# Optimization experiments

Hardware: AMD Instinct MI355X
Metric: run time of the kernel (lower is better)

## Reference

```python
import jax, jax.numpy as jnp
import numpy as np

NUM_HEADS = 16


def setup_inputs() -> dict:
    key = jax.random.key(0)
    kx, kp, kq, kw, kb = jax.random.split(key, 5)
    B, N, C = 2, 2048, 1024
    x = jax.random.normal(kx, (B, N, C), dtype=jnp.float32)
    padding_mask = jax.random.randint(kp, (B, N), 0, 2).astype(jnp.bool_)
    W_qkv = jax.random.normal(kq, (C, 3 * C), dtype=jnp.float32) * (C ** -0.5)
    W_proj = jax.random.normal(kw, (C, C), dtype=jnp.float32) * (C ** -0.5)
    b_proj = jax.random.normal(kb, (C,), dtype=jnp.float32) * 0.02
    return {"x": x, "padding_mask": padding_mask, "causal_start": 128,
            "W_qkv": W_qkv, "W_proj": W_proj, "b_proj": b_proj}


def reference(x, padding_mask, causal_start, W_qkv, W_proj, b_proj):
    B, N, C = x.shape
    H = NUM_HEADS
    d = C // H
    scale = d ** -0.5
    # qkv projection: (B,N,3C) -> (3,B,H,N,d)
    qkv = (x @ W_qkv).reshape(B, N, 3, H, d).transpose(2, 0, 3, 1, 4)
    q, k, v = qkv[0], qkv[1], qkv[2]
    attn = jnp.einsum("bhqd,bhkd->bhqk", q * scale, k)  # (B,H,N,N)
    # padding mask: mask out padded KEY positions
    attn = jnp.where(padding_mask[:, None, None, :], -jnp.inf, attn)
    # offset causal mask: lower-triangular, but first `causal_start` columns always visible
    allowed = jnp.tril(jnp.ones((N, N), dtype=jnp.bool_))
    allowed = allowed | (jnp.arange(N)[None, :] < causal_start)
    attn = jnp.where(~allowed[None, None, :, :], -jnp.inf, attn)
    attn = jax.nn.softmax(attn.astype(jnp.float32), axis=-1).astype(x.dtype)
    out = jnp.einsum("bhqk,bhkd->bhqd", attn, v)  # (B,H,N,d)
    out = out.transpose(0, 2, 1, 3).reshape(B, N, C)
    return out @ W_proj + b_proj
```

## Files before the change

kernel.cpp:

```cpp
#include <hip/hip_runtime.h>
#include <stdint.h>

typedef unsigned short ushort_t;
typedef __attribute__((ext_vector_type(4))) unsigned short ushort4_t;
typedef __attribute__((ext_vector_type(8))) short short8;
typedef __attribute__((ext_vector_type(4))) float float4_t;

#define AS1 __attribute__((address_space(1)))
#define AS3 __attribute__((address_space(3)))

__device__ inline ushort_t f2bf(float f) {
    unsigned x = __builtin_bit_cast(unsigned, f);
    unsigned r = x + 0x7fffu + ((x >> 16) & 1u);
    return (ushort_t)(r >> 16);
}
__device__ inline ushort_t f2bf_trunc(float f) {
    return (ushort_t)(__builtin_bit_cast(unsigned, f) >> 16);
}

__global__ __launch_bounds__(256) void prep_fused(
    const float* __restrict__ wqkv, const float* __restrict__ x,
    ushort_t* __restrict__ wqkvT, ushort_t* __restrict__ xbf) {
    __shared__ __align__(16) ushort_t tile[64][65];
    int bid = blockIdx.x, t = threadIdx.x;
    if (bid < 768) {
        int bx = bid % 48, by = bid / 48;
        int c0 = bx * 64, r0 = by * 64;
        for (int i = 0; i < 16; i++) {
            int idx = t + i * 256;
            int lr = idx >> 6, lc = idx & 63;
            tile[lr][lc] = f2bf(wqkv[(size_t)(r0 + lr) * 3072 + c0 + lc]);
        }
        __syncthreads();
        for (int i = 0; i < 16; i++) {
            int idx = t + i * 256;
            int lr = idx >> 6, lc = idx & 63;
            wqkvT[(size_t)(c0 + lr) * 1024 + r0 + lc] = tile[lc][lr];
        }
    } else {
        size_t i = ((size_t)(bid - 768) * 256 + t) * 8;
        float4_t a = *(const float4_t*)(x + i);
        float4_t b = *(const float4_t*)(x + i + 4);
        ushort_t u[8];
        u[0] = f2bf(a.x); u[1] = f2bf(a.y); u[2] = f2bf(a.z); u[3] = f2bf(a.w);
        u[4] = f2bf(b.x); u[5] = f2bf(b.y); u[6] = f2bf(b.z); u[7] = f2bf(b.w);
        *(ushort4_t*)(xbf + i) = *(ushort4_t*)&u[0];
        *(ushort4_t*)(xbf + i + 4) = *(ushort4_t*)&u[4];
    }
}

__global__ __launch_bounds__(256) void transpose_f32_bf16(const float* __restrict__ in,
                                                          ushort_t* __restrict__ out,
                                                          int R, int C) {
    __shared__ __align__(16) ushort_t tile[64][65];
    int c0 = blockIdx.x * 64, r0 = blockIdx.y * 64;
    int t = threadIdx.x;
    for (int i = 0; i < 16; i++) {
        int idx = t + i * 256;
        int lr = idx >> 6, lc = idx & 63;
        tile[lr][lc] = f2bf(in[(size_t)(r0 + lr) * C + c0 + lc]);
    }
    __syncthreads();
    for (int i = 0; i < 16; i++) {
        int idx = t + i * 256;
        int lr = idx >> 6, lc = idx & 63;
        out[(size_t)(c0 + lr) * R + r0 + lc] = tile[lc][lr];
    }
}

__global__ __launch_bounds__(256) void gemm_qkv(
    const ushort_t* __restrict__ A, const ushort_t* __restrict__ Bt,
    ushort_t* __restrict__ outQ, ushort_t* __restrict__ outK, ushort_t* __restrict__ outV) {
    const int K = 1024;
    __shared__ __align__(16) ushort_t As[128 * 64];
    __shared__ __align__(16) ushort_t Bs[128 * 64];
    int t = threadIdx.x;
    int w = t >> 6, lane = t & 63;
    int quad = lane >> 4, l15 = lane & 15;
    int wM = w >> 1, wN = w & 1;
    int tM = blockIdx.y * 128, tN = blockIdx.x * 128;

    float4_t acc[4][4];
    for (int i = 0; i < 4; i++)
        for (int j = 0; j < 4; j++) acc[i][j] = (float4_t){0.f, 0.f, 0.f, 0.f};

    int lrow = lane >> 3;
    int lcol8 = (lane & 7) * 8;

    const ushort_t* Abase = A + (size_t)(tM + w * 32) * K;
    const ushort_t* Bbase = Bt + (size_t)(tN + w * 32) * K;

    for (int k0 = 0; k0 < K; k0 += 64) {
        __syncthreads();
        for (int i = 0; i < 4; i++) {
            const ushort_t* ga = Abase + (size_t)(i * 8 + lrow) * K + k0 + lcol8;
            __builtin_amdgcn_global_load_lds((AS1 void*)ga, (AS3 void*)&As[(w * 32 + i * 8) * 64], 16, 0, 0);
            const ushort_t* gb = Bbase + (size_t)(i * 8 + lrow) * K + k0 + lcol8;
            __builtin_amdgcn_global_load_lds((AS1 void*)gb, (AS3 void*)&Bs[(w * 32 + i * 8) * 64], 16, 0, 0);
        }
        __syncthreads();
        for (int kt = 0; kt < 2; kt++) {
            short8 af[4], bf[4];
            for (int m = 0; m < 4; m++)
                af[m] = *(const short8*)&As[(wM * 64 + m * 16 + l15) * 64 + kt * 32 + quad * 8];
            for (int n = 0; n < 4; n++)
                bf[n] = *(const short8*)&Bs[(wN * 64 + n * 16 + l15) * 64 + kt * 32 + quad * 8];
            for (int m = 0; m < 4; m++)
                for (int n = 0; n < 4; n++)
                    acc[m][n] = __builtin_amdgcn_mfma_f32_16x16x32_bf16(af[m], bf[n], acc[m][n], 0, 0, 0);
        }
    }

    for (int m = 0; m < 4; m++) {
        int gm = tM + wM * 64 + m * 16 + quad * 4;
        for (int n = 0; n < 4; n++) {
            int gn = tN + wN * 64 + n * 16 + l15;
            int three = gn >> 10;
            int h = (gn >> 6) & 15;
            int dd = gn & 63;
            ushort_t* dst = (three == 0) ? outQ : (three == 1) ? outK : outV;
            for (int r = 0; r < 4; r++) {
                int row = gm + r;
                int b = row >> 11;
                int ns = row & 2047;
                dst[(((size_t)(b * 16 + h) * 2048 + ns) << 6) + dd] = f2bf(acc[m][n][r]);
            }
        }
    }
}

__global__ __launch_bounds__(512, 4) void attn_kernel(
    const ushort_t* __restrict__ q, const ushort_t* __restrict__ k,
    const ushort_t* __restrict__ v, const int* __restrict__ pad,
    const int* __restrict__ csp, ushort_t* __restrict__ out) {
    __shared__ __align__(16) ushort_t Ks[2][64 * 64];
    __shared__ __align__(16) ushort_t VsT[2][64 * 64];
    __shared__ __align__(16) ushort_t Ps[8][16 * 64];
    __shared__ float padb[2048];

    int cs = csp[0];
    int t = threadIdx.x, w = t >> 6, lane = t & 63;
    int quad = lane >> 4, l15 = lane & 15;
    int bh = blockIdx.y;
    int b = bh >> 4, h = bh & 15;
    int g = (blockIdx.y < 16) ? blockIdx.x : 15 - blockIdx.x;
    int q0 = g * 128;
    int rowmin = q0 + w * 16;
    const float c1 = 0.18033688f;
    const float c2 = -11.541560f;

    for (int i = 0; i < 4; i++) {
        int key = t + i * 512;
        padb[key] = pad[b * 2048 + key] ? -1e38f : c2;
    }

    const ushort_t* qb = q + ((size_t)bh * 2048 + rowmin + l15) * 64;
    short8 qf0 = *(const short8*)(qb + quad * 8);
    short8 qf1 = *(const short8*)(qb + 32 + quad * 8);

    float4_t O[4];
    for (int i = 0; i < 4; i++) O[i] = (float4_t){0.f, 0.f, 0.f, 0.f};
    float ls[4] = {0.f, 0.f, 0.f, 0.f};

    int csT = (cs + 63) >> 6;
    int nT = 2 * g + 2;
    if (csT > nT) nT = csT;

    const ushort_t* kbase = k + (size_t)bh * 2048 * 64;
    const ushort_t* vbase = v + (size_t)bh * 2048 * 64;

    int lrow = lane >> 3, lblk = lane & 7;
    int prow = rowmin + quad * 4;
    int sw = l15 & 7;

    short8 vr;
    auto stageK = [&](int it, int buf) {
        int k0 = it * 64;
        const ushort_t* gk = kbase + (size_t)(k0 + w * 8 + lrow) * 64 + ((lblk ^ lrow) * 8);
        __builtin_amdgcn_global_load_lds((AS1 void*)gk, (AS3 void*)&Ks[buf][w * 8 * 64], 16, 0, 0);
    };
    auto loadV = [&](int it) {
        vr = *(const short8*)(vbase + (size_t)(it * 64 + lane) * 64 + w * 8);
    };

    stageK(0, 0);
    loadV(0);

    for (int it = 0; it < nT; it++) {
        int cur = it & 1, nxt = cur ^ 1;
        for (int j = 0; j < 8; j++) {
            int sl = ((lrow ^ j) * 8) + lblk;
            VsT[cur][(w * 8 + j) * 64 + sl] = (ushort_t)vr[j];
        }
        __syncthreads();
        if (it + 1 < nT) {
            stageK(it + 1, nxt);
            loadV(it + 1);
        }

        int k0 = it * 64;
        bool act = (k0 <= rowmin + 15) || (k0 < cs);
        if (act) {
            short8 kf0[4], kf1[4];
            for (int ks = 0; ks < 4; ks++) {
                const ushort_t* krow = &Ks[cur][(ks * 16 + l15) * 64];
                kf0[ks] = *(const short8*)(krow + (quad ^ sw) * 8);
                kf1[ks] = *(const short8*)(krow + ((4 + quad) ^ sw) * 8);
            }

            float4_t s[4];
            for (int ks = 0; ks < 4; ks++) {
                float4_t a = (float4_t){0.f, 0.f, 0.f, 0.f};
                a = __builtin_amdgcn_mfma_f32_16x16x32_bf16(qf0, kf0[ks], a, 0, 0, 0);
                a = __builtin_amdgcn_mfma_f32_16x16x32_bf16(qf1, kf1[ks], a, 0, 0, 0);
                s[ks] = a;
            }
            bool needC = (k0 + 63 > rowmin) && (k0 + 63 >= cs);
            for (int ks = 0; ks < 4; ks++) {
                int key = k0 + ks * 16 + l15;
                float add = padb[key];
                for (int r = 0; r < 4; r++) {
                    float arg = s[ks][r] * c1 + add;
                    if (needC && (key > prow + r) && (key >= cs)) arg = -1e38f;
                    float p = __builtin_amdgcn_exp2f(arg);
                    ls[r] += p;
                    int row = quad * 4 + r;
                    Ps[w][row * 64 + (((ks * 2 + (l15 >> 3)) ^ (row & 7)) * 8) + (l15 & 7)] = f2bf_trunc(p);
                }
            }

            short8 vf0[4], vf1[4];
            for (int n = 0; n < 4; n++) {
                const ushort_t* vrow = &VsT[cur][(n * 16 + l15) * 64];
                vf0[n] = *(const short8*)(vrow + (quad ^ sw) * 8);
                vf1[n] = *(const short8*)(vrow + ((4 + quad) ^ sw) * 8);
            }
            const ushort_t* prl = &Ps[w][l15 * 64];
            short8 pf0 = *(const short8*)(prl + (quad ^ sw) * 8);
            short8 pf1 = *(const short8*)(prl + ((4 + quad) ^ sw) * 8);
            for (int n = 0; n < 4; n++) {
                O[n] = __builtin_amdgcn_mfma_f32_16x16x32_bf16(pf0, vf0[n], O[n], 0, 0, 0);
                O[n] = __builtin_amdgcn_mfma_f32_16x16x32_bf16(pf1, vf1[n], O[n], 0, 0, 0);
            }
        }
    }

    for (int r = 0; r < 4; r++) {
        float l = ls[r];
        l += __shfl_xor(l, 1, 64); l += __shfl_xor(l, 2, 64);
        l += __shfl_xor(l, 4, 64); l += __shfl_xor(l, 8, 64);
        float inv = l > 0.f ? 1.f / l : 0.f;
        int row = rowmin + quad * 4 + r;
        size_t ob = ((size_t)b * 2048 + row) * 1024 + h * 64;
        for (int n = 0; n < 4; n++)
            out[ob + n * 16 + l15] = f2bf(O[n][r] * inv);
    }
}

__global__ __launch_bounds__(256) void gemm_out_k(
    const ushort_t* __restrict__ A, const ushort_t* __restrict__ Bt,
    const float* __restrict__ bias, float* __restrict__ outC) {
    const int K = 1024, N = 1024;
    __shared__ __align__(16) ushort_t As[128 * 64];
    __shared__ __align__(16) ushort_t Bs[128 * 64];
    int t = threadIdx.x;
    int w = t >> 6, lane = t & 63;
    int quad = lane >> 4, l15 = lane & 15;
    int wM = w >> 1, wN = w & 1;
    int tM = blockIdx.y * 128, tN = blockIdx.x * 128;

    float4_t acc[4][4];
    for (int i = 0; i < 4; i++)
        for (int j = 0; j < 4; j++) acc[i][j] = (float4_t){0.f, 0.f, 0.f, 0.f};

    int lrow = lane >> 3;
    int lcol8 = (lane & 7) * 8;

    const ushort_t* Abase = A + (size_t)(tM + w * 32) * K;
    const ushort_t* Bbase = Bt + (size_t)(tN + w * 32) * K;

    for (int k0 = 0; k0 < K; k0 += 64) {
        __syncthreads();
        for (int i = 0; i < 4; i++) {
            const ushort_t* ga = Abase + (size_t)(i * 8 + lrow) * K + k0 + lcol8;
            __builtin_amdgcn_global_load_lds((AS1 void*)ga, (AS3 void*)&As[(w * 32 + i * 8) * 64], 16, 0, 0);
            const ushort_t* gb = Bbase + (size_t)(i * 8 + lrow) * K + k0 + lcol8;
            __builtin_amdgcn_global_load_lds((AS1 void*)gb, (AS3 void*)&Bs[(w * 32 + i * 8) * 64], 16, 0, 0);
        }
        __syncthreads();
        for (int kt = 0; kt < 2; kt++) {
            short8 af[4], bf[4];
            for (int m = 0; m < 4; m++)
                af[m] = *(const short8*)&As[(wM * 64 + m * 16 + l15) * 64 + kt * 32 + quad * 8];
            for (int n = 0; n < 4; n++)
                bf[n] = *(const short8*)&Bs[(wN * 64 + n * 16 + l15) * 64 + kt * 32 + quad * 8];
            for (int m = 0; m < 4; m++)
                for (int n = 0; n < 4; n++)
                    acc[m][n] = __builtin_amdgcn_mfma_f32_16x16x32_bf16(af[m], bf[n], acc[m][n], 0, 0, 0);
        }
    }

    for (int m = 0; m < 4; m++) {
        int gm = tM + wM * 64 + m * 16 + quad * 4;
        for (int n = 0; n < 4; n++) {
            int gn = tN + wN * 64 + n * 16 + l15;
            float bv = bias[gn];
            for (int r = 0; r < 4; r++)
                outC[(size_t)(gm + r) * N + gn] = acc[m][n][r] + bv;
        }
    }
}

extern "C" void kernel_launch(void* const* d_in, const int* in_sizes, int n_in,
                              void* d_out, int out_size, void* d_ws, size_t ws_size,
                              hipStream_t stream) {
    const float* x = (const float*)d_in[0];
    const int* pad = (const int*)d_in[1];
    const int* cs = (const int*)d_in[2];
    const float* wqkv = (const float*)d_in[3];
    const float* wproj = (const float*)d_in[4];
    const float* bproj = (const float*)d_in[5];
    float* out = (float*)d_out;

    ushort_t* ws = (ushort_t*)d_ws;
    ushort_t* qws = ws;
    ushort_t* kws = ws + (size_t)4194304;
    ushort_t* vws = ws + (size_t)8388608;
    ushort_t* wqkvT = ws + (size_t)12582912;
    ushort_t* aows = ws + (size_t)12582912;
    ushort_t* wprojT = ws;
    ushort_t* xbf = (ushort_t*)d_out;

    prep_fused<<<2816, 256, 0, stream>>>(wqkv, x, wqkvT, xbf);
    gemm_qkv<<<dim3(24, 32), 256, 0, stream>>>(xbf, wqkvT, qws, kws, vws);
    attn_kernel<<<dim3(16, 32), 512, 0, stream>>>(qws, kws, vws, pad, cs, aows);
    transpose_f32_bf16<<<dim3(16, 16), 256, 0, stream>>>(wproj, wprojT, 1024, 1024);
    gemm_out_k<<<dim3(8, 32), 256, 0, stream>>>(aows, wprojT, bproj, out);
}
```

Before: 201.0 us.

## Split long causal attention rows across blocks with atomic accumulation and combine pass

Result: slower. 258.3 us (+28.5%).

```diff
diff --git a/kernel.cpp b/kernel.cpp
--- a/kernel.cpp
+++ b/kernel.cpp
@@ -129,30 +129,36 @@
     }
 }
 
-__global__ __launch_bounds__(512, 4) void attn_kernel(
+__global__ __launch_bounds__(512, 6) void attn_kernel(
     const ushort_t* __restrict__ q, const ushort_t* __restrict__ k,
     const ushort_t* __restrict__ v, const int* __restrict__ pad,
-    const int* __restrict__ csp, ushort_t* __restrict__ out) {
+    const int* __restrict__ csp, ushort_t* __restrict__ out,
+    float* __restrict__ Oacc, float* __restrict__ lsacc) {
     __shared__ __align__(16) ushort_t Ks[2][64 * 64];
     __shared__ __align__(16) ushort_t VsT[2][64 * 64];
     __shared__ __align__(16) ushort_t Ps[8][16 * 64];
-    __shared__ float padb[2048];
+
+    const int g_tab[24]  = {0,1,2,3,8,8,4,9, 15,13,12,10,10,11,9,5, 15,7,14,14,6,12,13,11};
+    const int t0_tab[24] = {0,0,0,0,0,9,0,10, 0,0,0,0,11,0,0,0,    16,0,0,15,0,13,14,12};
+    const int t1_tab[24] = {2,4,6,8,9,18,10,20, 16,14,13,11,22,12,10,12, 32,16,15,30,14,26,28,24};
 
     int cs = csp[0];
     int t = threadIdx.x, w = t >> 6, lane = t & 63;
     int quad = lane >> 4, l15 = lane & 15;
     int bh = blockIdx.y;
     int b = bh >> 4, h = bh & 15;
-    int g = (blockIdx.y < 16) ? blockIdx.x : 15 - blockIdx.x;
+    int xi = blockIdx.x;
+    int g = g_tab[xi];
+    int it0 = t0_tab[xi], it1 = t1_tab[xi];
+    bool split = (g >= 8);
     int q0 = g * 128;
     int rowmin = q0 + w * 16;
     const float c1 = 0.18033688f;
     const float c2 = -11.541560f;
 
-    for (int i = 0; i < 4; i++) {
-        int key = t + i * 512;
-        padb[key] = pad[b * 2048 + key] ? -1e38f : c2;
-    }
+    int csT = (cs + 63) >> 6;
+    bool lastitem = (g < 8) || (it0 > 0);
+    if (lastitem && csT > it1) it1 = csT;
 
     const ushort_t* qb = q + ((size_t)bh * 2048 + rowmin + l15) * 64;
     short8 qf0 = *(const short8*)(qb + quad * 8);
@@ -162,12 +168,9 @@
     for (int i = 0; i < 4; i++) O[i] = (float4_t){0.f, 0.f, 0.f, 0.f};
     float ls[4] = {0.f, 0.f, 0.f, 0.f};
 
-    int csT = (cs + 63) >> 6;
-    int nT = 2 * g + 2;
-    if (csT > nT) nT = csT;
-
     const ushort_t* kbase = k + (size_t)bh * 2048 * 64;
     const ushort_t* vbase = v + (size_t)bh * 2048 * 64;
+    const int* padp = pad + b * 2048;
 
     int lrow = lane >> 3, lblk = lane & 7;
     int prow = rowmin + quad * 4;
@@ -183,17 +186,17 @@
         vr = *(const short8*)(vbase + (size_t)(it * 64 + lane) * 64 + w * 8);
     };
 
-    stageK(0, 0);
-    loadV(0);
-
-    for (int it = 0; it < nT; it++) {
+    stageK(it0, it0 & 1);
+    loadV(it0);
+
+    for (int it = it0; it < it1; it++) {
         int cur = it & 1, nxt = cur ^ 1;
         for (int j = 0; j < 8; j++) {
             int sl = ((lrow ^ j) * 8) + lblk;
             VsT[cur][(w * 8 + j) * 64 + sl] = (ushort_t)vr[j];
         }
         __syncthreads();
-        if (it + 1 < nT) {
+        if (it + 1 < it1) {
             stageK(it + 1, nxt);
             loadV(it + 1);
         }
@@ -201,6 +204,9 @@
         int k0 = it * 64;
         bool act = (k0 <= rowmin + 15) || (k0 < cs);
         if (act) {
+            int pvv[4];
+            for (int ks = 0; ks < 4; ks++) pvv[ks] = padp[k0 + ks * 16 + l15];
+
             short8 kf0[4], kf1[4];
             for (int ks = 0; ks < 4; ks++) {
                 const ushort_t* krow = &Ks[cur][(ks * 16 + l15) * 64];
@@ -218,7 +224,7 @@
             bool needC = (k0 + 63 > rowmin) && (k0 + 63 >= cs);
             for (int ks = 0; ks < 4; ks++) {
                 int key = k0 + ks * 16 + l15;
-                float add = padb[key];
+                float add = pvv[ks] ? -1e38f : c2;
                 for (int r = 0; r < 4; r++) {
                     float arg = s[ks][r] * c1 + add;
                     if (needC && (key > prow + r) && (key >= cs)) arg = -1e38f;
@@ -245,16 +251,47 @@
         }
     }
 
-    for (int r = 0; r < 4; r++) {
-        float l = ls[r];
-        l += __shfl_xor(l, 1, 64); l += __shfl_xor(l, 2, 64);
-        l += __shfl_xor(l, 4, 64); l += __shfl_xor(l, 8, 64);
-        float inv = l > 0.f ? 1.f / l : 0.f;
-        int row = rowmin + quad * 4 + r;
-        size_t ob = ((size_t)b * 2048 + row) * 1024 + h * 64;
-        for (int n = 0; n < 4; n++)
-            out[ob + n * 16 + l15] = f2bf(O[n][r] * inv);
-    }
+    if (!split) {
+        for (int r = 0; r < 4; r++) {
+            float l = ls[r];
+            l += __shfl_xor(l, 1, 64); l += __shfl_xor(l, 2, 64);
+            l += __shfl_xor(l, 4, 64); l += __shfl_xor(l, 8, 64);
+            float inv = l > 0.f ? 1.f / l : 0.f;
+            int row = rowmin + quad * 4 + r;
+            size_t ob = ((size_t)b * 2048 + row) * 1024 + h * 64;
+            for (int n = 0; n < 4; n++)
+                out[ob + n * 16 + l15] = f2bf(O[n][r] * inv);
+        }
+    } else {
+        for (int r = 0; r < 4; r++) {
+            float l = ls[r];
+            l += __shfl_xor(l, 1, 64); l += __shfl_xor(l, 2, 64);
+            l += __shfl_xor(l, 4, 64); l += __shfl_xor(l, 8, 64);
+            int row = rowmin + quad * 4 + r;
+            int rn = row - 1024;
+            if (l15 == 0) atomicAdd(&lsacc[bh * 1024 + rn], l);
+            float* orow = Oacc + ((size_t)(b * 1024 + rn)) * 1024 + h * 64;
+            for (int n = 0; n < 4; n++)
+                atomicAdd(&orow[n * 16 + l15], O[n][r]);
+        }
+    }
+}
+
+__global__ __launch_bounds__(256) void combine_norm(
+    const float* __restrict__ Oacc, const float* __restrict__ lsacc,
+    ushort_t* __restrict__ aows) {
+    int rid = blockIdx.x;
+    int b = rid >> 10, rn = rid & 1023;
+    int c0 = threadIdx.x * 4;
+    const float* orow = Oacc + (size_t)rid * 1024;
+    float4_t o = *(const float4_t*)(orow + c0);
+    int h = c0 >> 6;
+    float l = lsacc[(b * 16 + h) * 1024 + rn];
+    float inv = l > 0.f ? 1.f / l : 0.f;
+    ushort_t u[4];
+    u[0] = f2bf(o.x * inv); u[1] = f2bf(o.y * inv);
+    u[2] = f2bf(o.z * inv); u[3] = f2bf(o.w * inv);
+    *(ushort4_t*)(aows + ((size_t)(b * 2048 + 1024 + rn)) * 1024 + c0) = *(ushort4_t*)u;
 }
 
 __global__ __launch_bounds__(256) void gemm_out_k(
@@ -330,10 +367,14 @@
     ushort_t* aows = ws + (size_t)12582912;
     ushort_t* wprojT = ws;
     ushort_t* xbf = (ushort_t*)d_out;
+    float* Oacc = (float*)d_out;
+    float* lsacc = (float*)d_out + 2097152;
 
     prep_fused<<<2816, 256, 0, stream>>>(wqkv, x, wqkvT, xbf);
     gemm_qkv<<<dim3(24, 32), 256, 0, stream>>>(xbf, wqkvT, qws, kws, vws);
-    attn_kernel<<<dim3(16, 32), 512, 0, stream>>>(qws, kws, vws, pad, cs, aows);
+    hipMemsetAsync(d_out, 0, (size_t)(2097152 + 32768) * 4, stream);
+    attn_kernel<<<dim3(24, 32), 512, 0, stream>>>(qws, kws, vws, pad, cs, aows, Oacc, lsacc);
     transpose_f32_bf16<<<dim3(16, 16), 256, 0, stream>>>(wproj, wprojT, 1024, 1024);
+    combine_norm<<<2048, 256, 0, stream>>>(Oacc, lsacc, aows);
     gemm_out_k<<<dim3(8, 32), 256, 0, stream>>>(aows, wprojT, bproj, out);
 }
```

## Compact padded keys out of K/V so attention skips masked tiles

Applied to the files above, without the earlier changes.

Result: no change. 200.1 us (-0.4%).

```diff
diff --git a/kernel.cpp b/kernel.cpp
--- a/kernel.cpp
+++ b/kernel.cpp
@@ -20,8 +20,11 @@
 
 __global__ __launch_bounds__(256) void prep_fused(
     const float* __restrict__ wqkv, const float* __restrict__ x,
-    ushort_t* __restrict__ wqkvT, ushort_t* __restrict__ xbf) {
+    const int* __restrict__ pad,
+    ushort_t* __restrict__ wqkvT, ushort_t* __restrict__ xbf,
+    int* __restrict__ tbl) {
     __shared__ __align__(16) ushort_t tile[64][65];
+    __shared__ int wsum[4];
     int bid = blockIdx.x, t = threadIdx.x;
     if (bid < 768) {
         int bx = bid % 48, by = bid / 48;
@@ -37,7 +40,7 @@
             int lr = idx >> 6, lc = idx & 63;
             wqkvT[(size_t)(c0 + lr) * 1024 + r0 + lc] = tile[lc][lr];
         }
-    } else {
+    } else if (bid < 2816) {
         size_t i = ((size_t)(bid - 768) * 256 + t) * 8;
         float4_t a = *(const float4_t*)(x + i);
         float4_t b = *(const float4_t*)(x + i + 4);
@@ -46,6 +49,40 @@
         u[4] = f2bf(b.x); u[5] = f2bf(b.y); u[6] = f2bf(b.z); u[7] = f2bf(b.w);
         *(ushort4_t*)(xbf + i) = *(ushort4_t*)&u[0];
         *(ushort4_t*)(xbf + i + 4) = *(ushort4_t*)&u[4];
+    } else {
+        int b = bid - 2816;
+        int* cvtab = tbl;
+        int* pref = tbl + 4096;
+        int* idxmap = tbl + 8192;
+        int* vcp = tbl + 12288;
+        int lane = t & 63, w4 = t >> 6;
+        int base0 = t * 8;
+        int v[8], s8 = 0;
+        for (int j = 0; j < 8; j++) {
+            v[j] = (pad[b * 2048 + base0 + j] == 0) ? 1 : 0;
+            s8 += v[j];
+        }
+        int incl = s8;
+        for (int off = 1; off < 64; off <<= 1) {
+            int y = __shfl_up(incl, off, 64);
+            if (lane >= off) incl += y;
+        }
+        int excl = incl - s8;
+        if (lane == 63) wsum[w4] = incl;
+        __syncthreads();
+        int wbase = 0;
+        for (int ww = 0; ww < 4; ww++) if (ww < w4) wbase += wsum[ww];
+        int vcall = wsum[0] + wsum[1] + wsum[2] + wsum[3];
+        int run = wbase + excl;
+        for (int j = 0; j < 8; j++) {
+            int pos = base0 + j;
+            pref[b * 2048 + pos] = run;
+            cvtab[b * 2048 + pos] = v[j] ? run : -1;
+            if (v[j]) idxmap[b * 2048 + run] = pos;
+            run += v[j];
+        }
+        if (t == 0) vcp[b] = vcall;
+        for (int s = vcall + t; s < 2048; s += 256) idxmap[b * 2048 + s] = 2048;
     }
 }
 
@@ -70,6 +107,7 @@
 
 __global__ __launch_bounds__(256) void gemm_qkv(
     const ushort_t* __restrict__ A, const ushort_t* __restrict__ Bt,
+    const int* __restrict__ cvtab,
     ushort_t* __restrict__ outQ, ushort_t* __restrict__ outK, ushort_t* __restrict__ outV) {
     const int K = 1024;
     __shared__ __align__(16) ushort_t As[128 * 64];
@@ -113,17 +151,27 @@
 
     for (int m = 0; m < 4; m++) {
         int gm = tM + wM * 64 + m * 16 + quad * 4;
+        int cvv[4];
+        for (int r = 0; r < 4; r++) cvv[r] = cvtab[gm + r];
         for (int n = 0; n < 4; n++) {
             int gn = tN + wN * 64 + n * 16 + l15;
             int three = gn >> 10;
             int h = (gn >> 6) & 15;
             int dd = gn & 63;
-            ushort_t* dst = (three == 0) ? outQ : (three == 1) ? outK : outV;
             for (int r = 0; r < 4; r++) {
                 int row = gm + r;
                 int b = row >> 11;
-                int ns = row & 2047;
-                dst[(((size_t)(b * 16 + h) * 2048 + ns) << 6) + dd] = f2bf(acc[m][n][r]);
+                ushort_t val = f2bf(acc[m][n][r]);
+                if (three == 0) {
+                    int ns = row & 2047;
+                    outQ[(((size_t)(b * 16 + h) * 2048 + ns) << 6) + dd] = val;
+                } else {
+                    int slot = cvv[r];
+                    if (slot >= 0) {
+                        ushort_t* dst = (three == 1) ? outK : outV;
+                        dst[(((size_t)(b * 16 + h) * 2048 + slot) << 6) + dd] = val;
+                    }
+                }
             }
         }
     }
@@ -131,12 +179,16 @@
 
 __global__ __launch_bounds__(512, 4) void attn_kernel(
     const ushort_t* __restrict__ q, const ushort_t* __restrict__ k,
-    const ushort_t* __restrict__ v, const int* __restrict__ pad,
+    const ushort_t* __restrict__ v, const int* __restrict__ tbl,
     const int* __restrict__ csp, ushort_t* __restrict__ out) {
     __shared__ __align__(16) ushort_t Ks[2][64 * 64];
     __shared__ __align__(16) ushort_t VsT[2][64 * 64];
     __shared__ __align__(16) ushort_t Ps[8][16 * 64];
-    __shared__ float padb[2048];
+    __shared__ int Idx[2048];
+
+    const int* pref = tbl + 4096;
+    const int* idxmap = tbl + 8192;
+    const int* vcp = tbl + 12288;
 
     int cs = csp[0];
     int t = threadIdx.x, w = t >> 6, lane = t & 63;
@@ -149,10 +201,11 @@
     const float c1 = 0.18033688f;
     const float c2 = -11.541560f;
 
-    for (int i = 0; i < 4; i++) {
-        int key = t + i * 512;
-        padb[key] = pad[b * 2048 + key] ? -1e38f : c2;
-    }
+    int bound = q0 + 128; if (cs > bound) bound = cs;
+    int nvalid = (bound > 2047) ? vcp[b] : pref[b * 2048 + bound];
+    int nT = (nvalid + 63) >> 6; if (nT < 1) nT = 1;
+
+    for (int i = 0; i < 4; i++) Idx[t + i * 512] = idxmap[b * 2048 + t + i * 512];
 
     const ushort_t* qb = q + ((size_t)bh * 2048 + rowmin + l15) * 64;
     short8 qf0 = *(const short8*)(qb + quad * 8);
@@ -161,10 +214,6 @@
     float4_t O[4];
     for (int i = 0; i < 4; i++) O[i] = (float4_t){0.f, 0.f, 0.f, 0.f};
     float ls[4] = {0.f, 0.f, 0.f, 0.f};
-
-    int csT = (cs + 63) >> 6;
-    int nT = 2 * g + 2;
-    if (csT > nT) nT = csT;
 
     const ushort_t* kbase = k + (size_t)bh * 2048 * 64;
     const ushort_t* vbase = v + (size_t)bh * 2048 * 64;
@@ -181,6 +230,8 @@
     };
     auto loadV = [&](int it) {
         vr = *(const short8*)(vbase + (size_t)(it * 64 + lane) * 64 + w * 8);
+        if (it * 64 + lane >= nvalid)
+            for (int j = 0; j < 8; j++) vr[j] = 0;
     };
 
     stageK(0, 0);
@@ -199,8 +250,12 @@
         }
 
         int k0 = it * 64;
-        bool act = (k0 <= rowmin + 15) || (k0 < cs);
+        int omin = Idx[k0];
+        bool act = (omin <= rowmin + 15) || (omin < cs);
         if (act) {
+            int omax = Idx[k0 + 63];
+            bool needC = (omax > rowmin) && (omax >= cs);
+
             short8 kf0[4], kf1[4];
             for (int ks = 0; ks < 4; ks++) {
                 const ushort_t* krow = &Ks[cur][(ks * 16 + l15) * 64];
@@ -215,12 +270,10 @@
                 a = __builtin_amdgcn_mfma_f32_16x16x32_bf16(qf1, kf1[ks], a, 0, 0, 0);
                 s[ks] = a;
             }
-            bool needC = (k0 + 63 > rowmin) && (k0 + 63 >= cs);
             for (int ks = 0; ks < 4; ks++) {
-                int key = k0 + ks * 16 + l15;
-                float add = padb[key];
+                int key = Idx[k0 + ks * 16 + l15];
                 for (int r = 0; r < 4; r++) {
-                    float arg = s[ks][r] * c1 + add;
+                    float arg = s[ks][r] * c1 + c2;
                     if (needC && (key > prow + r) && (key >= cs)) arg = -1e38f;
                     float p = __builtin_amdgcn_exp2f(arg);
                     ls[r] += p;
@@ -330,10 +383,11 @@
     ushort_t* aows = ws + (size_t)12582912;
     ushort_t* wprojT = ws;
     ushort_t* xbf = (ushort_t*)d_out;
-
-    prep_fused<<<2816, 256, 0, stream>>>(wqkv, x, wqkvT, xbf);
-    gemm_qkv<<<dim3(24, 32), 256, 0, stream>>>(xbf, wqkvT, qws, kws, vws);
-    attn_kernel<<<dim3(16, 32), 512, 0, stream>>>(qws, kws, vws, pad, cs, aows);
+    int* tbl = (int*)((char*)d_out + 8388608);
+
+    prep_fused<<<2818, 256, 0, stream>>>(wqkv, x, pad, wqkvT, xbf, tbl);
+    gemm_qkv<<<dim3(24, 32), 256, 0, stream>>>(xbf, wqkvT, tbl, qws, kws, vws);
+    attn_kernel<<<dim3(16, 32), 512, 0, stream>>>(qws, kws, vws, tbl, cs, aows);
     transpose_f32_bf16<<<dim3(16, 16), 256, 0, stream>>>(wproj, wprojT, 1024, 1024);
     gemm_out_k<<<dim3(8, 32), 256, 0, stream>>>(aows, wprojT, bproj, out);
 }
```
